# Kernel optimization log

Measured on AMD Instinct MI355X. Metric: run time of the kernel, lower is better.

The kernel has to match this reference:

```python
import jax, jax.numpy as jnp
import numpy as np
from jax import lax

B, N, G, K, D = 16, 8192, 256, 64, 256
DEPTH, H, HID, PH = 4, 8, 1024, 128
EPS = 1e-5
BN_SCALE = float(1.0 / np.sqrt(1.0 + 1e-5))  # BatchNorm eval, running mean 0 / var 1


def setup_inputs() -> dict:
    key = jax.random.key(0)
    ks = iter(jax.random.split(key, 48))
    def rn(shape, s=0.02):
        return jax.random.normal(next(ks), shape, jnp.float32) * s
    z = lambda *s: jnp.zeros(s, jnp.float32)
    o = lambda *s: jnp.ones(s, jnp.float32)
    return dict(
        x=jax.random.normal(next(ks), (B, N, 3), jnp.float32),
        enc_w1=rn((3, 128)), enc_b1=z(128), enc_bn1_g=o(128), enc_bn1_b=z(128),
        enc_w2=rn((128, 256)), enc_b2=z(256),
        enc_w3=rn((512, 512)), enc_b3=z(512), enc_bn2_g=o(512), enc_bn2_b=z(512),
        enc_w4=rn((512, D)), enc_b4=z(D),
        cls_token=rn((1, 1, D)), cls_pos=rn((1, 1, D)),
        pos_w1=rn((3, 128)), pos_b1=z(128), pos_w2=rn((128, D)), pos_b2=z(D),
        ln1_g=o(DEPTH, D), ln1_b=z(DEPTH, D),
        qkv_w=rn((DEPTH, D, 3 * D)),
        proj_w=rn((DEPTH, D, D)), proj_b=z(DEPTH, D),
        ln2_g=o(DEPTH, D), ln2_b=z(DEPTH, D),
        fc1_w=rn((DEPTH, D, HID)), fc1_b=z(DEPTH, HID),
        fc2_w=rn((DEPTH, HID, D)), fc2_b=z(DEPTH, D),
        norm_g=o(D), norm_b=z(D),
        head_w1=rn((D + 3, PH)), head_b1=z(PH), head_w2=rn((PH, 1)), head_b2=z(1),
    )


def layernorm(t, g, b):
    m = jnp.mean(t, -1, keepdims=True)
    v = jnp.mean((t - m) ** 2, -1, keepdims=True)
    return (t - m) / jnp.sqrt(v + EPS) * g + b


def fps(xyz, num_group):
    # farthest point sampling; deterministic start at index 0 (torch uses randint)
    Bb, Nn, _ = xyz.shape
    def body(i, st):
        dist, far, idxs = st
        idxs = idxs.at[:, i].set(far)
        cen = jnp.take_along_axis(xyz, far[:, None, None], axis=1)  # (B,1,3)
        d = jnp.sum((xyz - cen) ** 2, -1)
        dist = jnp.minimum(dist, d)
        far = jnp.argmax(dist, axis=1).astype(jnp.int32)
        return (dist, far, idxs)
    st0 = (jnp.full((Bb, Nn), 1e10, jnp.float32),
           jnp.zeros((Bb,), jnp.int32),
           jnp.zeros((Bb, num_group), jnp.int32))
    _, _, idxs = lax.fori_loop(0, num_group, body, st0)
    centers = jnp.take_along_axis(xyz, idxs[..., None], axis=1)  # (B,G,3)
    return centers, idxs


def knn(xyz, centers, k):
    # squared-distance cdist (same argsort order as p=2) + topk smallest
    c2 = jnp.sum(centers ** 2, -1)[:, :, None]
    x2 = jnp.sum(xyz ** 2, -1)[:, None, :]
    d2 = c2 + x2 - 2.0 * jnp.einsum('bgd,bnd->bgn', centers, xyz)  # (B,G,N)
    idx = lax.top_k(-d2, k)[1]  # (B,G,k)
    neigh = jax.vmap(lambda p, i: p[i])(xyz, idx)  # (B,G,k,3)
    return idx, neigh


def _forward(x, enc_w1, enc_b1, enc_bn1_g, enc_bn1_b, enc_w2, enc_b2,
             enc_w3, enc_b3, enc_bn2_g, enc_bn2_b, enc_w4, enc_b4,
             cls_token, cls_pos, pos_w1, pos_b1, pos_w2, pos_b2,
             ln1_g, ln1_b, qkv_w, proj_w, proj_b, ln2_g, ln2_b,
             fc1_w, fc1_b, fc2_w, fc2_b, norm_g, norm_b,
             head_w1, head_b1, head_w2, head_b2):
    Bb, Nn, _ = x.shape
    # grouping is @torch.no_grad() in the original -> stop_gradient
    pts = lax.stop_gradient(x)
    centers, _ = fps(pts, G)
    idx, neigh = knn(pts, centers, K)
    neigh = neigh - centers[:, :, None, :]  # (B,G,K,3) centered

    # PointNet encoder (kernel-size-1 convs == matmuls; BN eval with unit stats)
    pg = neigh.reshape(Bb * G, K, 3)
    h = pg @ enc_w1 + enc_b1                                # (BG,K,128)
    h = jax.nn.relu(h * enc_bn1_g * BN_SCALE + enc_bn1_b)
    h = h @ enc_w2 + enc_b2                                 # (BG,K,256)
    gmax = jnp.max(h, axis=1, keepdims=True)                # (BG,1,256)
    h = jnp.concatenate([jnp.broadcast_to(gmax, h.shape), h], -1)  # (BG,K,512)
    h = h @ enc_w3 + enc_b3
    h = jax.nn.relu(h * enc_bn2_g * BN_SCALE + enc_bn2_b)
    h = h @ enc_w4 + enc_b4                                 # (BG,K,D)
    tokens = jnp.max(h, axis=1).reshape(Bb, G, D)

    pos = jax.nn.gelu(centers @ pos_w1 + pos_b1, approximate=False) @ pos_w2 + pos_b2
    xt = jnp.concatenate([jnp.broadcast_to(cls_token, (Bb, 1, D)), tokens], 1)
    pt = jnp.concatenate([jnp.broadcast_to(cls_pos, (Bb, 1, D)), pos], 1)

    scale = (D // H) ** -0.5
    for l in range(DEPTH):
        xi = xt + pt  # pos added before every block
        h1 = layernorm(xi, ln1_g[l], ln1_b[l])
        qkv = (h1 @ qkv_w[l]).reshape(Bb, G + 1, 3, H, D // H).transpose(2, 0, 3, 1, 4)
        q, k_, v = qkv[0], qkv[1], qkv[2]
        attn = jax.nn.softmax(jnp.einsum('bhnd,bhmd->bhnm', q, k_) * scale, -1)
        o = jnp.einsum('bhnm,bhmd->bhnd', attn, v).transpose(0, 2, 1, 3).reshape(Bb, G + 1, D)
        xi = xi + o @ proj_w[l] + proj_b[l]
        h2 = layernorm(xi, ln2_g[l], ln2_b[l])
        xi = xi + jax.nn.gelu(h2 @ fc1_w[l] + fc1_b[l], approximate=False) @ fc2_w[l] + fc2_b[l]
        xt = xi
    xt = layernorm(xt, norm_g, norm_b)

    gfeat = xt[:, 1:, :]  # (B,G,D)
    concat = jnp.concatenate(
        [jnp.broadcast_to(gfeat[:, :, None, :], (Bb, G, K, D)), neigh], -1)  # (B,G,K,D+3)
    lg = (jax.nn.relu(concat @ head_w1 + head_b1) @ head_w2 + head_b2)[..., 0]  # (B,G,K)

    # scatter-mean per-point logits over original N points
    flat_i = idx.reshape(Bb, G * K)
    flat_v = lg.reshape(Bb, G * K)
    sums = jax.vmap(lambda v, i: jax.ops.segment_sum(v, i, num_segments=N))(flat_v, flat_i)
    cnts = jax.vmap(lambda i: jax.ops.segment_sum(jnp.ones(i.shape, jnp.float32), i, num_segments=N))(flat_i)
    return sums / jnp.maximum(cnts, 1.0)  # (B,N)


def reference(x, enc_w1, enc_b1, enc_bn1_g, enc_bn1_b, enc_w2, enc_b2,
              enc_w3, enc_b3, enc_bn2_g, enc_bn2_b, enc_w4, enc_b4,
              cls_token, cls_pos, pos_w1, pos_b1, pos_w2, pos_b2,
              ln1_g, ln1_b, qkv_w, proj_w, proj_b, ln2_g, ln2_b,
              fc1_w, fc1_b, fc2_w, fc2_b, norm_g, norm_b,
              head_w1, head_b1, head_w2, head_b2):
    return _forward(x, enc_w1, enc_b1, enc_bn1_g, enc_bn1_b, enc_w2, enc_b2,
                    enc_w3, enc_b3, enc_bn2_g, enc_bn2_b, enc_w4, enc_b4,
                    cls_token, cls_pos, pos_w1, pos_b1, pos_w2, pos_b2,
                    ln1_g, ln1_b, qkv_w, proj_w, proj_b, ln2_g, ln2_b,
                    fc1_w, fc1_b, fc2_w, fc2_b, norm_g, norm_b,
                    head_w1, head_b1, head_w2, head_b2)
```

## Files before the change

### kernel.cpp

```cpp
#include <hip/hip_runtime.h>
#include <hip/hip_bf16.h>

#define B_ 16
#define N_ 8192
#define G_ 256
#define K_ 64
#define D_ 256
#define HID_ 1024
#define EPS_ 1e-5f

typedef __attribute__((ext_vector_type(8))) short bf16x8;
typedef __attribute__((ext_vector_type(4))) float f32x4;

__device__ __forceinline__ float bf16_to_f32(unsigned short u){
  unsigned int v = ((unsigned int)u) << 16;
  return __uint_as_float(v);
}
__device__ __forceinline__ unsigned short f32_to_bf16(float f){
  unsigned int u = __float_as_uint(f);
  unsigned int r = (u + 0x7FFFu + ((u >> 16) & 1u)) >> 16;
  return (unsigned short)r;
}
__device__ __forceinline__ unsigned short bf16h(float a){
  __hip_bfloat16 h = __float2bfloat16(a);
  union { __hip_bfloat16 h; unsigned short u; } cv; cv.h = h; return cv.u;
}
__device__ __forceinline__ unsigned int pk_bf16(float a, float b){
  __hip_bfloat162 h = __float22bfloat162_rn(make_float2(a, b));
  union { __hip_bfloat162 h; unsigned int u; } cv; cv.h = h; return cv.u;
}
__device__ __forceinline__ float gelu_exact(float v){
  return 0.5f * v * (1.0f + erff(v * 0.70710678118654752440f));
}

template<int CTRL>
__device__ __forceinline__ unsigned long long dpp64(unsigned long long k){
  int lo = (int)(unsigned int)k;
  int hi = (int)(unsigned int)(k >> 32);
  int dlo = __builtin_amdgcn_update_dpp(lo, lo, CTRL, 0xF, 0xF, false);
  int dhi = __builtin_amdgcn_update_dpp(hi, hi, CTRL, 0xF, 0xF, false);
  return (((unsigned long long)(unsigned int)dhi) << 32) | (unsigned int)dlo;
}
__device__ __forceinline__ unsigned long long bcast64(unsigned long long k, int lane){
  unsigned int lo = (unsigned int)__builtin_amdgcn_readlane((int)(unsigned int)k, lane);
  unsigned int hi = (unsigned int)__builtin_amdgcn_readlane((int)(unsigned int)(k >> 32), lane);
  return (((unsigned long long)hi) << 32) | lo;
}
__device__ __forceinline__ unsigned long long wave_max64(unsigned long long k){
  unsigned long long t;
  t = dpp64<0x111>(k); if (t > k) k = t;
  t = dpp64<0x112>(k); if (t > k) k = t;
  t = dpp64<0x114>(k); if (t > k) k = t;
  t = dpp64<0x118>(k); if (t > k) k = t;
  t = dpp64<0x142>(k); if (t > k) k = t;
  t = dpp64<0x143>(k); if (t > k) k = t;
  return bcast64(k, 63);
}
__device__ __forceinline__ unsigned long long wave_min64(unsigned long long k){
  unsigned long long t;
  t = dpp64<0x111>(k); if (t < k) k = t;
  t = dpp64<0x112>(k); if (t < k) k = t;
  t = dpp64<0x114>(k); if (t < k) k = t;
  t = dpp64<0x118>(k); if (t < k) k = t;
  t = dpp64<0x142>(k); if (t < k) k = t;
  t = dpp64<0x143>(k); if (t < k) k = t;
  return bcast64(k, 63);
}
__device__ __forceinline__ unsigned long long red8_max64(unsigned long long k){
  unsigned long long t;
  t = dpp64<0x111>(k); if (t > k) k = t;
  t = dpp64<0x112>(k); if (t > k) k = t;
  t = dpp64<0x114>(k); if (t > k) k = t;
  return bcast64(k, 7);
}
__device__ __forceinline__ unsigned long long red4_min64(unsigned long long k){
  unsigned long long t;
  t = dpp64<0x111>(k); if (t < k) k = t;
  t = dpp64<0x112>(k); if (t < k) k = t;
  return bcast64(k, 3);
}

__device__ __forceinline__ void packHi(const float* __restrict__ W, unsigned short* __restrict__ hi,
                                       int f, int N, int ksBits){
  int j = f & 7, lane = (f >> 3) & 63;
  int ks = (f >> 9) & ((1 << ksBits) - 1);
  int nt = f >> (9 + ksBits);
  int k = ks * 32 + ((lane >> 4) & 3) * 8 + j, c = nt * 16 + (lane & 15);
  hi[f] = f32_to_bf16(W[(size_t)k * N + c]);
}

__global__ __launch_bounds__(512) void prep_fps_kernel(
    const float* __restrict__ x, float* __restrict__ centers,
    const float* __restrict__ w1, const float* __restrict__ b1,
    const float* __restrict__ g1, const float* __restrict__ bb1,
    const float* __restrict__ w3, const float* __restrict__ b3,
    const float* __restrict__ g2, const float* __restrict__ bb2,
    const float* __restrict__ enc_w2, const float* __restrict__ enc_w4,
    const float* __restrict__ qkv_w, const float* __restrict__ proj_w,
    const float* __restrict__ fc1_w, const float* __restrict__ fc2_w,
    float* __restrict__ w1f, float* __restrict__ b1f, float* __restrict__ b3f,
    unsigned short* __restrict__ w2ph, unsigned short* __restrict__ w2pl,
    unsigned short* __restrict__ w3ph, unsigned short* __restrict__ w4ph,
    unsigned short* __restrict__ qkvPh, unsigned short* __restrict__ projPh,
    unsigned short* __restrict__ fc1Ph, unsigned short* __restrict__ fc2Ph,
    unsigned short* __restrict__ w3tp)
{
  const float S = 0.99999500003749968f;
  int blk = blockIdx.x, tid = threadIdx.x;

  if (blk >= 17){
    int f = (blk - 17) * 512 + tid;
    if (f < 32768){
      int j = f & 7, lane = (f >> 3) & 63, ks = (f >> 9) & 3, nt = f >> 11;
      int k = ks * 32 + ((lane >> 4) & 3) * 8 + j, c = nt * 16 + (lane & 15);
      float v = enc_w2[(size_t)k * 256 + c];
      unsigned short h = f32_to_bf16(v);
      w2ph[f] = h; w2pl[f] = f32_to_bf16(v - bf16_to_f32(h));
    } else if (f < 163840){
      f -= 32768;
      int j = f & 7, lane = (f >> 3) & 63, ks = (f >> 9) & 7, nt = f >> 12;
      int k = ks * 32 + ((lane >> 4) & 3) * 8 + j, c = nt * 16 + (lane & 15);
      w3ph[f] = f32_to_bf16(w3[(size_t)(256 + k) * 512 + c] * g2[c] * S);
    } else if (f < 294912){
      f -= 163840;
      packHi(enc_w4, w4ph, f, 256, 4);
    } else if (f < 1081344){
      f -= 294912;
      int l = f / 196608, fl = f - l * 196608;
      packHi(qkv_w + (size_t)l * 196608, qkvPh + (size_t)l * 196608, fl, 768, 3);
    } else if (f < 1343488){
      f -= 1081344;
      int l = f >> 16, fl = f & 65535;
      packHi(proj_w + (size_t)l * 65536, projPh + (size_t)l * 65536, fl, 256, 3);
    } else if (f < 2392064){
      f -= 1343488;
      int l = f >> 18, fl = f & 262143;
      packHi(fc1_w + (size_t)l * 262144, fc1Ph + (size_t)l * 262144, fl, 1024, 3);
    } else if (f < 3440640){
      f -= 2392064;
      int l = f >> 18, fl = f & 262143;
      packHi(fc2_w + (size_t)l * 262144, fc2Ph + (size_t)l * 262144, fl, 256, 5);
    } else {
      f -= 3440640;
      int j = f & 7, lane = (f >> 3) & 63, ks = (f >> 9) & 7, nt = f >> 12;
      int k = ks * 32 + ((lane >> 4) & 3) * 8 + j, c = nt * 16 + (lane & 15);
      w3tp[f] = f32_to_bf16(w3[(size_t)k * 512 + c] * g2[c] * S);
    }
    return;
  }
  if (blk == 16){
    if (tid < 384) w1f[tid] = w1[tid] * g1[tid & 127] * S;
    if (tid < 128) b1f[tid] = b1[tid] * g1[tid] * S + bb1[tid];
    b3f[tid] = b3[tid] * g2[tid] * S + bb2[tid];
    return;
  }

  int b = blk;
  const float* xb = x + (size_t)b * N_ * 3;
  int lane = tid & 63, wave = tid >> 6;
  float px[16], py[16], pz[16], dist[16];
#pragma unroll
  for (int j = 0; j < 16; j++){
    int p = tid + j * 512;
    px[j] = xb[p*3+0]; py[j] = xb[p*3+1]; pz[j] = xb[p*3+2];
    dist[j] = 1e10f;
  }
  __shared__ unsigned long long slotK[2][8];
  __shared__ float slotC[2][8][4];
  float cx = xb[0], cy = xb[1], cz = xb[2];
  for (int i = 0; i < G_; i++){
    if (tid == 0){
      float* cp = centers + ((size_t)b * G_ + i) * 3;
      cp[0] = cx; cp[1] = cy; cp[2] = cz;
    }
    float bestv = -1.0f; int bestj = 0;
#pragma unroll
    for (int j = 0; j < 16; j++){
      float dx = __fadd_rn(px[j], -cx);
      float dy = __fadd_rn(py[j], -cy);
      float dz = __fadd_rn(pz[j], -cz);
      float d  = __fadd_rn(__fadd_rn(__fmul_rn(dx,dx), __fmul_rn(dy,dy)), __fmul_rn(dz,dz));
      float dm = fminf(dist[j], d);
      dist[j] = dm;
      if (dm > bestv){ bestv = dm; bestj = j; }
    }
    unsigned int pid = (unsigned int)(tid + bestj * 512);
    unsigned long long key = (((unsigned long long)__float_as_uint(bestv)) << 32) | (unsigned long long)(~pid);
    key = wave_max64(key);
    int par = i & 1;
    unsigned int wpid = ~(unsigned int)key;
    if (lane == (int)(wpid & 63)){
      int jj = (int)(wpid >> 9);
      float fx = px[0], fy = py[0], fz = pz[0];
#pragma unroll
      for (int j = 1; j < 16; j++) if (jj == j){ fx = px[j]; fy = py[j]; fz = pz[j]; }
      slotK[par][wave] = key;
      slotC[par][wave][0] = fx; slotC[par][wave][1] = fy; slotC[par][wave][2] = fz;
    }
    __syncthreads();
    if (i + 1 < G_){
      unsigned long long k2 = slotK[par][lane & 7];
      k2 = red8_max64(k2);
      unsigned int gpid = ~(unsigned int)k2;
      int s = (int)((gpid & 511u) >> 6);
      cx = slotC[par][s][0]; cy = slotC[par][s][1]; cz = slotC[par][s][2];
    }
  }
}

__global__ __launch_bounds__(256) void knn_kernel(const float* __restrict__ x, const float* __restrict__ centers,
                                                  int* __restrict__ knn_idx, float* __restrict__ neigh)
{
  int blk = blockIdx.x, b = blk >> 8;
  const float* xb = x + (size_t)b * N_ * 3;
  const float* cc = centers + (size_t)blk * 3;
  int tid = threadIdx.x, lane = tid & 63, wave = tid >> 6;
  float c0 = cc[0], c1 = cc[1], c2v = cc[2];
  float c2s = __fadd_rn(__fadd_rn(__fmul_rn(c0,c0), __fmul_rn(c1,c1)), __fmul_rn(c2v,c2v));
  float d[32];
#pragma unroll
  for (int j = 0; j < 32; j++){
    int p = tid + j * 256;
    float x0 = xb[p*3+0], x1 = xb[p*3+1], x2 = xb[p*3+2];
    float xs = __fadd_rn(__fadd_rn(__fmul_rn(x0,x0), __fmul_rn(x1,x1)), __fmul_rn(x2,x2));
    float dt = __fadd_rn(__fadd_rn(__fmul_rn(c0,x0), __fmul_rn(c1,x1)), __fmul_rn(c2v,x2));
    d[j] = __fadd_rn(__fadd_rn(c2s, xs), -__fmul_rn(2.0f, dt));
  }
  const float FINF = __int_as_float(0x7F800000);
  float lmin = FINF; unsigned int lp = 0xFFFFFFFFu;
#pragma unroll
  for (int j = 0; j < 32; j++){ if (d[j] < lmin){ lmin = d[j]; lp = (unsigned int)(tid + j*256); } }
  __shared__ unsigned long long wred[2][4];
  for (int r = 0; r < K_; r++){
    unsigned int u = __float_as_uint(lmin);
    u = (u & 0x80000000u) ? ~u : (u | 0x80000000u);
    unsigned long long key = (((unsigned long long)u) << 32) | (unsigned long long)lp;
    key = wave_min64(key);
    int cur = r & 1;
    if (lane == 0) wred[cur][wave] = key;
    __syncthreads();
    unsigned long long m = red4_min64(wred[cur][lane & 3]);
    unsigned int p = (unsigned int)(m & 0xFFFFFFFFull);
    if (tid == (p & 255u)){
      knn_idx[(size_t)blk * K_ + r] = (int)p;
      float* np_ = neigh + ((size_t)blk * K_ + r) * 3;
      np_[0] = __fadd_rn(xb[p*3+0], -c0);
      np_[1] = __fadd_rn(xb[p*3+1], -c1);
      np_[2] = __fadd_rn(xb[p*3+2], -c2v);
      lmin = FINF; lp = 0xFFFFFFFFu;
#pragma unroll
      for (int j = 0; j < 32; j++){
        if ((unsigned int)(tid + j*256) == p) d[j] = FINF;
        if (d[j] < lmin){ lmin = d[j]; lp = (unsigned int)(tid + j*256); }
      }
    }
  }
}

__global__ __launch_bounds__(256, 2) void encoder_kernel(
    const float* __restrict__ neigh,
    const float* __restrict__ w1f, const float* __restrict__ b1f,
    const unsigned short* __restrict__ w2ph, const unsigned short* __restrict__ w2pl,
    const float* __restrict__ b2,
    const float* __restrict__ b3f,
    const unsigned short* __restrict__ w3ph, const unsigned short* __restrict__ w3tp,
    const unsigned short* __restrict__ w4ph,
    const float* __restrict__ b4,
    float* __restrict__ tokens)
{
  __shared__ __align__(16) unsigned short sH1[64 * 136];
  __shared__ __align__(16) unsigned short sH2[64 * 264];
  __shared__ __align__(16) float sShared[256];
  float (*sNeigh)[4] = (float(*)[4])sShared;
  unsigned short* sGmaxBf = (unsigned short*)sShared;

  int tid  = threadIdx.x;
  int wave = tid >> 6, lane = tid & 63, quad = lane >> 4, lrow = lane & 15;
  size_t gid = blockIdx.x;

  if (tid < 192) sNeigh[tid / 3][tid % 3] = neigh[gid * 192 + tid];
  __syncthreads();

  for (int e = tid; e < 8192; e += 256){
    int r = e >> 7, c = e & 127;
    float v = fmaf(sNeigh[r][2], w1f[256 + c], fmaf(sNeigh[r][1], w1f[128 + c], fmaf(sNeigh[r][0], w1f[c], b1f[c])));
    sH1[r * 136 + c] = bf16h(fmaxf(v, 0.0f));
  }
  __syncthreads();

  {
    f32x4 acc[4][4];
    const f32x4 z = {0.f, 0.f, 0.f, 0.f};
#pragma unroll
    for (int mt = 0; mt < 4; mt++)
#pragma unroll
      for (int nl = 0; nl < 4; nl++) acc[mt][nl] = z;
#pragma unroll
    for (int ks = 0; ks < 4; ks++){
      bf16x8 af[4];
#pragma unroll
      for (int mt = 0; mt < 4; mt++)
        af[mt] = *(const bf16x8*)&sH1[(mt*16 + lrow)*136 + ks*32 + quad*8];
#pragma unroll
      for (int nl = 0; nl < 4; nl++){
        size_t bo = (((size_t)(wave*4 + nl)*4 + ks)*64 + lane)*8;
        bf16x8 bh = *(const bf16x8*)&w2ph[bo];
        bf16x8 bl = *(const bf16x8*)&w2pl[bo];
#pragma unroll
        for (int mt = 0; mt < 4; mt++){
          acc[mt][nl] = __builtin_amdgcn_mfma_f32_16x16x32_bf16(af[mt], bh, acc[mt][nl], 0, 0, 0);
          acc[mt][nl] = __builtin_amdgcn_mfma_f32_16x16x32_bf16(af[mt], bl, acc[mt][nl], 0, 0, 0);
        }
      }
    }
#pragma unroll
    for (int nl = 0; nl < 4; nl++){
      int col = wave*64 + nl*16 + lrow;
      float bias = b2[col];
#pragma unroll
      for (int mt = 0; mt < 4; mt++)
#pragma unroll
        for (int rg = 0; rg < 4; rg++)
          sH2[(mt*16 + quad*4 + rg)*264 + col] = bf16h(acc[mt][nl][rg] + bias);
    }
  }
  __syncthreads();

  {
    float mx = -3.4e38f;
#pragma unroll 8
    for (int r = 0; r < 64; r++) mx = fmaxf(mx, bf16_to_f32(sH2[r*264 + tid]));
    sGmaxBf[tid] = bf16h(mx);
  }
  __syncthreads();

  f32x4 acc4[4][4];
  {
    const f32x4 z = {0.f, 0.f, 0.f, 0.f};
#pragma unroll
    for (int mt = 0; mt < 4; mt++)
#pragma unroll
      for (int nl = 0; nl < 4; nl++) acc4[mt][nl] = z;
  }
  for (int cc = 0; cc < 4; cc++){
    f32x4 acc3[4][2], accg[2];
    {
      const f32x4 z = {0.f, 0.f, 0.f, 0.f};
#pragma unroll
      for (int mt = 0; mt < 4; mt++){ acc3[mt][0] = z; acc3[mt][1] = z; }
      accg[0] = z; accg[1] = z;
    }
#pragma unroll
    for (int ks = 0; ks < 8; ks++){
      bf16x8 gf = *(const bf16x8*)&sGmaxBf[ks*32 + quad*8];
#pragma unroll
      for (int nl = 0; nl < 2; nl++){
        int nt = cc*8 + wave*2 + nl;
        size_t bo = (((size_t)nt*8 + ks)*64 + lane)*8;
        bf16x8 bh = *(const bf16x8*)&w3tp[bo];
        accg[nl] = __builtin_amdgcn_mfma_f32_16x16x32_bf16(gf, bh, accg[nl], 0, 0, 0);
      }
    }
#pragma unroll
    for (int ks = 0; ks < 8; ks++){
      bf16x8 af[4];
#pragma unroll
      for (int mt = 0; mt < 4; mt++)
        af[mt] = *(const bf16x8*)&sH2[(mt*16 + lrow)*264 + ks*32 + quad*8];
#pragma unroll
      for (int nl = 0; nl < 2; nl++){
        int nt = cc*8 + wave*2 + nl;
        size_t bo = (((size_t)nt*8 + ks)*64 + lane)*8;
        bf16x8 bh = *(const bf16x8*)&w3ph[bo];
#pragma unroll
        for (int mt = 0; mt < 4; mt++)
          acc3[mt][nl] = __builtin_amdgcn_mfma_f32_16x16x32_bf16(af[mt], bh, acc3[mt][nl], 0, 0, 0);
      }
    }
    __syncthreads();
#pragma unroll
    for (int nl = 0; nl < 2; nl++){
      int cl = wave*32 + nl*16 + lrow;
      int c  = cc*128 + cl;
      float bb = b3f[c];
#pragma unroll
      for (int mt = 0; mt < 4; mt++)
#pragma unroll
        for (int rg = 0; rg < 4; rg++)
          sH1[(mt*16 + quad*4 + rg)*136 + cl] = bf16h(fmaxf(acc3[mt][nl][rg] + accg[nl][rg] + bb, 0.0f));
    }
    __syncthreads();
#pragma unroll
    for (int ks = 0; ks < 4; ks++){
      bf16x8 af[4];
#pragma unroll
      for (int mt = 0; mt < 4; mt++)
        af[mt] = *(const bf16x8*)&sH1[(mt*16 + lrow)*136 + ks*32 + quad*8];
#pragma unroll
      for (int nl = 0; nl < 4; nl++){
        int nt = wave*4 + nl;
        size_t bo = (((size_t)nt*16 + cc*4 + ks)*64 + lane)*8;
        bf16x8 bh = *(const bf16x8*)&w4ph[bo];
#pragma unroll
        for (int mt = 0; mt < 4; mt++)
          acc4[mt][nl] = __builtin_amdgcn_mfma_f32_16x16x32_bf16(af[mt], bh, acc4[mt][nl], 0, 0, 0);
      }
    }
  }

#pragma unroll
  for (int nl = 0; nl < 4; nl++){
    float mx = -3.4e38f;
#pragma unroll
    for (int mt = 0; mt < 4; mt++)
#pragma unroll
      for (int rg = 0; rg < 4; rg++) mx = fmaxf(mx, acc4[mt][nl][rg]);
    mx = fmaxf(mx, __shfl_xor(mx, 16));
    mx = fmaxf(mx, __shfl_xor(mx, 32));
    if (quad == 0){
      int col = wave*64 + nl*16 + lrow;
      tokens[gid * 256 + col] = mx + b4[col];
    }
  }
}

__global__ __launch_bounds__(128) void pos_ln_kernel(
    const float* __restrict__ centers, const float* __restrict__ tokens,
    const float* __restrict__ cls_token, const float* __restrict__ cls_pos,
    const float* __restrict__ pw1, const float* __restrict__ pb1,
    const float* __restrict__ pw2, const float* __restrict__ pb2,
    const float* __restrict__ lng, const float* __restrict__ lnb,
    float* __restrict__ pt, float* __restrict__ xi, float* __restrict__ lnbuf)
{
  __shared__ float hS[128];
  __shared__ float red[2][2];
  int row = blockIdx.x;
  int b = row / 257, n = row - b * 257;
  int tid = threadIdx.x;
  size_t ro = (size_t)row * 256;
  float u0, u1;
  if (n == 0){
    float p0 = cls_pos[tid], p1 = cls_pos[128 + tid];
    u0 = cls_token[tid] + p0; u1 = cls_token[128 + tid] + p1;
    pt[ro + tid] = p0; pt[ro + 128 + tid] = p1;
  } else {
    int g = n - 1;
    const float* c = centers + ((size_t)b * 256 + g) * 3;
    float h = fmaf(c[2], pw1[256 + tid], fmaf(c[1], pw1[128 + tid], fmaf(c[0], pw1[tid], pb1[tid])));
    hS[tid] = gelu_exact(h);
    __syncthreads();
    const float* tok = tokens + ((size_t)b * 256 + g) * 256;
    float s0 = pb2[tid], s1 = pb2[128 + tid];
#pragma unroll 4
    for (int k = 0; k < 128; k++){
      s0 = fmaf(hS[k], pw2[(size_t)k * 256 + tid], s0);
      s1 = fmaf(hS[k], pw2[(size_t)k * 256 + 128 + tid], s1);
    }
    pt[ro + tid] = s0; pt[ro + 128 + tid] = s1;
    u0 = tok[tid] + s0; u1 = tok[128 + tid] + s1;
  }
  float s = u0 + u1, q = u0*u0 + u1*u1;
#pragma unroll
  for (int o = 32; o; o >>= 1){ s += __shfl_down(s, o); q += __shfl_down(q, o); }
  int wv = tid >> 6;
  if ((tid & 63) == 0){ red[0][wv] = s; red[1][wv] = q; }
  __syncthreads();
  float m  = (red[0][0] + red[0][1]) * (1.0f / 256.0f);
  float var = (red[1][0] + red[1][1]) * (1.0f / 256.0f) - m * m;
  float rs = 1.0f / sqrtf(var + EPS_);
  xi[ro + tid] = u0; xi[ro + 128 + tid] = u1;
  lnbuf[ro + tid] = (u0 - m) * rs * lng[tid] + lnb[tid];
  lnbuf[ro + 128 + tid] = (u1 - m) * rs * lng[128 + tid] + lnb[128 + tid];
}

template<int ACT>
__global__ __launch_bounds__(256) void mfma_gemm(
    const float* __restrict__ A, const unsigned short* __restrict__ Bh,
    const float* __restrict__ bias, float* __restrict__ C, int M, int K, int N)
{
  __shared__ __align__(16) unsigned short sA[64 * 72];
  int tid = threadIdx.x;
  int wave = tid >> 6, lane = tid & 63, quad = lane >> 4, lrow = lane & 15;
  int row0 = blockIdx.x * 64;
  int col0 = blockIdx.y * 128;
  int ksTotal = K >> 5;
  f32x4 acc[4][2];
  const f32x4 z = {0.f, 0.f, 0.f, 0.f};
#pragma unroll
  for (int mt = 0; mt < 4; mt++){ acc[mt][0] = z; acc[mt][1] = z; }

  for (int k0 = 0; k0 < K; k0 += 64){
#pragma unroll
    for (int i = 0; i < 4; i++){
      int e = tid + i * 256;
      int r = e >> 4, c4 = (e & 15) * 4;
      int gr = row0 + r;
      float4 v = make_float4(0.f,0.f,0.f,0.f);
      if (gr < M) v = *(const float4*)(A + (size_t)gr * K + k0 + c4);
      unsigned int* dst = (unsigned int*)&sA[r * 72 + c4];
      dst[0] = pk_bf16(v.x, v.y); dst[1] = pk_bf16(v.z, v.w);
    }
    __syncthreads();
    int ksBase = k0 >> 5;
#pragma unroll
    for (int ks = 0; ks < 2; ks++){
      bf16x8 af[4];
#pragma unroll
      for (int mt = 0; mt < 4; mt++)
        af[mt] = *(const bf16x8*)&sA[(mt*16 + lrow)*72 + ks*32 + quad*8];
#pragma unroll
      for (int nl = 0; nl < 2; nl++){
        int nt = (col0 >> 4) + wave*2 + nl;
        size_t bo = (((size_t)nt * ksTotal + ksBase + ks)*64 + lane)*8;
        bf16x8 bh = *(const bf16x8*)&Bh[bo];
#pragma unroll
        for (int mt = 0; mt < 4; mt++)
          acc[mt][nl] = __builtin_amdgcn_mfma_f32_16x16x32_bf16(af[mt], bh, acc[mt][nl], 0, 0, 0);
      }
    }
    __syncthreads();
  }
#pragma unroll
  for (int nl = 0; nl < 2; nl++){
    int c = col0 + wave*32 + nl*16 + lrow;
    float bc = bias ? bias[c] : 0.0f;
#pragma unroll
    for (int mt = 0; mt < 4; mt++)
#pragma unroll
      for (int rg = 0; rg < 4; rg++){
        int r = row0 + mt*16 + quad*4 + rg;
        if (r < M){
          float v = acc[mt][nl][rg] + bc;
          if (ACT == 1) v = gelu_exact(v);
          C[(size_t)r * N + c] = v;
        }
      }
  }
}

__global__ __launch_bounds__(256) void mfma_gemm_ln(
    const float* __restrict__ A, const unsigned short* __restrict__ Bh,
    const float* __restrict__ bias, const float* __restrict__ res,
    const float* __restrict__ ptb,
    float* __restrict__ C, float* __restrict__ xiOut, float* __restrict__ lnOut,
    const float* __restrict__ lng, const float* __restrict__ lnb, int M, int K)
{
  __shared__ __align__(16) unsigned short sA[64 * 72];
  __shared__ float sRed[2][64][4];
  int tid = threadIdx.x;
  int wave = tid >> 6, lane = tid & 63, quad = lane >> 4, lrow = lane & 15;
  int row0 = blockIdx.x * 64;
  int ksTotal = K >> 5;
  f32x4 acc[4][4];
  const f32x4 z = {0.f, 0.f, 0.f, 0.f};
#pragma unroll
  for (int mt = 0; mt < 4; mt++)
#pragma unroll
    for (int nl = 0; nl < 4; nl++) acc[mt][nl] = z;

  for (int k0 = 0; k0 < K; k0 += 64){
#pragma unroll
    for (int i = 0; i < 4; i++){
      int e = tid + i * 256;
      int r = e >> 4, c4 = (e & 15) * 4;
      int gr = row0 + r;
      float4 v = make_float4(0.f,0.f,0.f,0.f);
      if (gr < M) v = *(const float4*)(A + (size_t)gr * K + k0 + c4);
      unsigned int* dst = (unsigned int*)&sA[r * 72 + c4];
      dst[0] = pk_bf16(v.x, v.y); dst[1] = pk_bf16(v.z, v.w);
    }
    __syncthreads();
    int ksBase = k0 >> 5;
#pragma unroll
    for (int ks = 0; ks < 2; ks++){
      bf16x8 af[4];
#pragma unroll
      for (int mt = 0; mt < 4; mt++)
        af[mt] = *(const bf16x8*)&sA[(mt*16 + lrow)*72 + ks*32 + quad*8];
#pragma unroll
      for (int nl = 0; nl < 4; nl++){
        int nt = wave*4 + nl;
        size_t bo = (((size_t)nt * ksTotal + ksBase + ks)*64 + lane)*8;
        bf16x8 bh = *(const bf16x8*)&Bh[bo];
#pragma unroll
        for (int mt = 0; mt < 4; mt++)
          acc[mt][nl] = __builtin_amdgcn_mfma_f32_16x16x32_bf16(af[mt], bh, acc[mt][nl], 0, 0, 0);
      }
    }
    __syncthreads();
  }
#pragma unroll
  for (int nl = 0; nl < 4; nl++){
    int c = wave*64 + nl*16 + lrow;
    float bc = bias[c];
#pragma unroll
    for (int mt = 0; mt < 4; mt++)
#pragma unroll
      for (int rg = 0; rg < 4; rg++){
        int r = row0 + mt*16 + quad*4 + rg;
        if (r < M){
          float v = acc[mt][nl][rg] + bc + res[(size_t)r * 256 + c];
          C[(size_t)r * 256 + c] = v;
          float u = v;
          if (ptb) u += ptb[(size_t)r * 256 + c];
          acc[mt][nl][rg] = u;
        }
      }
  }
#pragma unroll
  for (int mt = 0; mt < 4; mt++)
#pragma unroll
    for (int rg = 0; rg < 4; rg++){
      int rloc = mt*16 + quad*4 + rg;
      float s = 0.0f, q = 0.0f;
#pragma unroll
      for (int nl = 0; nl < 4; nl++){ float u = acc[mt][nl][rg]; s += u; q += u*u; }
#pragma unroll
      for (int off = 1; off < 16; off <<= 1){ s += __shfl_xor(s, off); q += __shfl_xor(q, off); }
      if (lrow == 0){ sRed[0][rloc][wave] = s; sRed[1][rloc][wave] = q; }
    }
  __syncthreads();
#pragma unroll
  for (int mt = 0; mt < 4; mt++)
#pragma unroll
    for (int rg = 0; rg < 4; rg++){
      int rloc = mt*16 + quad*4 + rg;
      int r = row0 + rloc;
      if (r >= M) continue;
      float s = ((sRed[0][rloc][0] + sRed[0][rloc][1]) + sRed[0][rloc][2]) + sRed[0][rloc][3];
      float q = ((sRed[1][rloc][0] + sRed[1][rloc][1]) + sRed[1][rloc][2]) + sRed[1][rloc][3];
      float m  = s * (1.0f / 256.0f);
      float var = q * (1.0f / 256.0f) - m * m;
      float rs = 1.0f / sqrtf(var + EPS_);
#pragma unroll
      for (int nl = 0; nl < 4; nl++){
        int c = wave*64 + nl*16 + lrow;
        float u = acc[mt][nl][rg];
        lnOut[(size_t)r * 256 + c] = (u - m) * rs * lng[c] + lnb[c];
        if (xiOut) xiOut[(size_t)r * 256 + c] = u;
      }
    }
}

__global__ __launch_bounds__(256) void attn_kernel(const float* __restrict__ qkv, float* __restrict__ obuf)
{
  int bh = blockIdx.x;
  int b = bh >> 3, h = bh & 7;
  int tid = threadIdx.x;
  int qi = tid >> 2, kp = tid & 3;
  int qrow = blockIdx.y * 64 + qi;
  bool act = qrow < 257;
  __shared__ float kS[128][33];
  __shared__ float vS[128][33];
  const float* qb = qkv + (size_t)b * 257 * 768;
  float q[32], o[32];
  float mrun = -3.4e38f, l = 0.0f;
  if (act){
    const float* qr = qb + (size_t)qrow * 768 + h * 32;
#pragma unroll
    for (int j = 0; j < 32; j++){ q[j] = qr[j]; o[j] = 0.0f; }
  }
  const float scale = 0.17677669529663687f;
  for (int m0 = 0; m0 < 257; m0 += 128){
    int cnt = min(128, 257 - m0);
    for (int e = tid; e < cnt * 32; e += 256){
      int mm = e >> 5, j = e & 31;
      const float* rowp = qb + (size_t)(m0 + mm) * 768 + h * 32;
      kS[mm][j] = rowp[256 + j];
      vS[mm][j] = rowp[512 + j];
    }
    __syncthreads();
    if (act){
      for (int mm = kp; mm < cnt; mm += 4){
        float s = 0.0f;
#pragma unroll
        for (int j = 0; j < 32; j++) s = fmaf(q[j], kS[mm][j], s);
        s *= scale;
        float nm = fmaxf(mrun, s);
        float alpha = expf(mrun - nm);
        float p = expf(s - nm);
        l = fmaf(l, alpha, p);
#pragma unroll
        for (int j = 0; j < 32; j++) o[j] = fmaf(p, vS[mm][j], o[j] * alpha);
        mrun = nm;
      }
    }
    __syncthreads();
  }
  if (act){
#pragma unroll
    for (int msk = 1; msk <= 2; msk <<= 1){
      float m2 = __shfl_xor(mrun, msk);
      float l2 = __shfl_xor(l, msk);
      float nm = fmaxf(mrun, m2);
      float a1 = expf(mrun - nm), a2 = expf(m2 - nm);
      l = l * a1 + l2 * a2;
#pragma unroll
      for (int j = 0; j < 32; j++){
        float o2 = __shfl_xor(o[j], msk);
        o[j] = o[j] * a1 + o2 * a2;
      }
      mrun = nm;
    }
    if (kp == 0){
      float inv = 1.0f / l;
      float* orow = obuf + (size_t)(b * 257 + qrow) * 256 + h * 32;
#pragma unroll
      for (int j = 0; j < 32; j++) orow[j] = o[j] * inv;
    }
  }
}

__global__ __launch_bounds__(256) void head_kernel(
    const float* __restrict__ gfeat, const float* __restrict__ neigh, const int* __restrict__ knn_idx,
    const float* __restrict__ w1, const float* __restrict__ b1,
    const float* __restrict__ w2, const float* __restrict__ b2,
    float* __restrict__ sums, float* __restrict__ cnts)
{
  int blk = blockIdx.x, b = blk >> 8;
  __shared__ float xS[256];
  __shared__ float nS[64][4];
  __shared__ float partH[2][128];
  __shared__ float sharedH[128];
  __shared__ float w2S[128];
  __shared__ float wtail[3][128];
  int tid = threadIdx.x;
  xS[tid] = gfeat[((size_t)b * 257 + 1 + (blk & 255)) * 256 + tid];
  if (tid < 192) nS[tid / 3][tid % 3] = neigh[(size_t)blk * 192 + tid];
  if (tid < 128){
    w2S[tid] = w2[tid];
    wtail[0][tid] = w1[256 * 128 + tid];
    wtail[1][tid] = w1[257 * 128 + tid];
    wtail[2][tid] = w1[258 * 128 + tid];
  }
  __syncthreads();
  {
    int half = tid >> 7, j = tid & 127;
    float s = 0.0f;
#pragma unroll 8
    for (int k = 0; k < 128; k++) s = fmaf(xS[half * 128 + k], w1[(size_t)(half * 128 + k) * 128 + j], s);
    partH[half][j] = s;
  }
  __syncthreads();
  if (tid < 128) sharedH[tid] = partH[0][tid] + partH[1][tid] + b1[tid];
  __syncthreads();
  int r = tid >> 2, q = tid & 3;
  float n0 = nS[r][0], n1 = nS[r][1], n2 = nS[r][2];
  float s = 0.0f;
#pragma unroll
  for (int j0 = 0; j0 < 32; j0++){
    int j = q * 32 + j0;
    float h = fmaf(n2, wtail[2][j], fmaf(n1, wtail[1][j], fmaf(n0, wtail[0][j], sharedH[j])));
    s = fmaf(fmaxf(h, 0.0f), w2S[j], s);
  }
  s += __shfl_xor(s, 1);
  s += __shfl_xor(s, 2);
  if (q == 0){
    float lg = s + b2[0];
    int p = knn_idx[(size_t)blk * K_ + r];
    atomicAdd(&sums[(size_t)b * N_ + p], lg);
    atomicAdd(&cnts[(size_t)b * N_ + p], 1.0f);
  }
}

__global__ void finalize_kernel(const float* __restrict__ sums, const float* __restrict__ cnts, float* __restrict__ out)
{
  int i = blockIdx.x * 256 + threadIdx.x;
  out[i] = sums[i] / fmaxf(cnts[i], 1.0f);
}

extern "C" void kernel_launch(void* const* d_in, const int* in_sizes, int n_in,
                              void* d_out, int out_size, void* d_ws, size_t ws_size,
                              hipStream_t stream)
{
  (void)in_sizes; (void)n_in; (void)out_size; (void)ws_size;
  const float* x        = (const float*)d_in[0];
  const float* enc_w1   = (const float*)d_in[1];
  const float* enc_b1   = (const float*)d_in[2];
  const float* enc_bn1g = (const float*)d_in[3];
  const float* enc_bn1b = (const float*)d_in[4];
  const float* enc_w2   = (const float*)d_in[5];
  const float* enc_b2   = (const float*)d_in[6];
  const float* enc_w3   = (const float*)d_in[7];
  const float* enc_b3   = (const float*)d_in[8];
  const float* enc_bn2g = (const float*)d_in[9];
  const float* enc_bn2b = (const float*)d_in[10];
  const float* enc_w4   = (const float*)d_in[11];
  const float* enc_b4   = (const float*)d_in[12];
  const float* cls_tok  = (const float*)d_in[13];
  const float* cls_pos  = (const float*)d_in[14];
  const float* pos_w1   = (const float*)d_in[15];
  const float* pos_b1   = (const float*)d_in[16];
  const float* pos_w2   = (const float*)d_in[17];
  const float* pos_b2   = (const float*)d_in[18];
  const float* ln1_g    = (const float*)d_in[19];
  const float* ln1_b    = (const float*)d_in[20];
  const float* qkv_w    = (const float*)d_in[21];
  const float* proj_w   = (const float*)d_in[22];
  const float* proj_b   = (const float*)d_in[23];
  const float* ln2_g    = (const float*)d_in[24];
  const float* ln2_b    = (const float*)d_in[25];
  const float* fc1_w    = (const float*)d_in[26];
  const float* fc1_b    = (const float*)d_in[27];
  const float* fc2_w    = (const float*)d_in[28];
  const float* fc2_b    = (const float*)d_in[29];
  const float* norm_g   = (const float*)d_in[30];
  const float* norm_b   = (const float*)d_in[31];
  const float* head_w1  = (const float*)d_in[32];
  const float* head_b1  = (const float*)d_in[33];
  const float* head_w2  = (const float*)d_in[34];
  const float* head_b2  = (const float*)d_in[35];

  float* ws = (float*)d_ws;
  size_t off = 0;
  auto alloc = [&](size_t n)->float*{ float* p = ws + off; off += (n + 63) & ~(size_t)63; return p; };

  float* centers = alloc((size_t)B_ * G_ * 3);
  float* w1f     = alloc(384);
  float* b1f     = alloc(128);
  float* b3f     = alloc(512);
  unsigned short* w2ph = (unsigned short*)alloc(16384);
  unsigned short* w2pl = (unsigned short*)alloc(16384);
  unsigned short* w3ph = (unsigned short*)alloc(65536);
  unsigned short* w3tp = (unsigned short*)alloc(65536);
  unsigned short* w4ph = (unsigned short*)alloc(65536);
  unsigned short* qkvPh = (unsigned short*)alloc(393216);
  unsigned short* projPh = (unsigned short*)alloc(131072);
  unsigned short* fc1Ph = (unsigned short*)alloc(524288);
  unsigned short* fc2Ph = (unsigned short*)alloc(524288);
  float* tokens  = alloc((size_t)B_ * G_ * D_);
  float* neigh   = alloc((size_t)B_ * G_ * K_ * 3);
  int*   knn_idx = (int*)alloc((size_t)B_ * G_ * K_);
  float* pt      = alloc((size_t)B_ * 257 * D_);
  float* xt      = alloc((size_t)B_ * 257 * D_);
  float* xi      = alloc((size_t)B_ * 257 * D_);
  float* lnbuf   = alloc((size_t)B_ * 257 * D_);
  float* obuf    = alloc((size_t)B_ * 257 * D_);
  float* bigbuf  = alloc((size_t)B_ * 257 * HID_);
  float* gfeat   = alloc((size_t)B_ * 257 * D_);
  float* sums    = alloc((size_t)B_ * N_);
  float* cnts    = alloc((size_t)B_ * N_);

  hipMemsetAsync(sums, 0, (size_t)2 * B_ * N_ * sizeof(float), stream);

  prep_fps_kernel<<<6993, 512, 0, stream>>>(x, centers,
      enc_w1, enc_b1, enc_bn1g, enc_bn1b, enc_w3, enc_b3, enc_bn2g, enc_bn2b,
      enc_w2, enc_w4, qkv_w, proj_w, fc1_w, fc2_w,
      w1f, b1f, b3f, w2ph, w2pl, w3ph, w4ph, qkvPh, projPh, fc1Ph, fc2Ph, w3tp);

  knn_kernel<<<B_ * G_, 256, 0, stream>>>(x, centers, knn_idx, neigh);
  encoder_kernel<<<B_ * G_, 256, 0, stream>>>(neigh, w1f, b1f, w2ph, w2pl, enc_b2,
                                              b3f, w3ph, w3tp, w4ph, enc_b4, tokens);
  pos_ln_kernel<<<B_ * 257, 128, 0, stream>>>(centers, tokens, cls_tok, cls_pos,
                                              pos_w1, pos_b1, pos_w2, pos_b2,
                                              ln1_g, ln1_b, pt, xi, lnbuf);
  const int M = B_ * 257;
  for (int l = 0; l < 4; l++){
    mfma_gemm<0><<<dim3(65, 6), 256, 0, stream>>>(lnbuf, qkvPh + (size_t)l*196608, nullptr, bigbuf, M, 256, 768);
    attn_kernel<<<dim3(B_ * 8, 5), 256, 0, stream>>>(bigbuf, obuf);
    mfma_gemm_ln<<<65, 256, 0, stream>>>(obuf, projPh + (size_t)l*65536, proj_b + l*256, xi, nullptr,
                                         xi, nullptr, lnbuf, ln2_g + l*256, ln2_b + l*256, M, 256);
    mfma_gemm<1><<<dim3(65, 8), 256, 0, stream>>>(lnbuf, fc1Ph + (size_t)l*262144, fc1_b + l*1024, bigbuf, M, 256, 1024);
    if (l < 3){
      mfma_gemm_ln<<<65, 256, 0, stream>>>(bigbuf, fc2Ph + (size_t)l*262144, fc2_b + l*256, xi, pt,
                                           xt, xi, lnbuf, ln1_g + (l+1)*256, ln1_b + (l+1)*256, M, 1024);
    } else {
      mfma_gemm_ln<<<65, 256, 0, stream>>>(bigbuf, fc2Ph + (size_t)l*262144, fc2_b + l*256, xi, nullptr,
                                           xt, nullptr, gfeat, norm_g, norm_b, M, 1024);
    }
  }
  head_kernel<<<B_ * G_, 256, 0, stream>>>(gfeat, neigh, knn_idx, head_w1, head_b1, head_w2, head_b2, sums, cnts);
  finalize_kernel<<<(B_ * N_) / 256, 256, 0, stream>>>(sums, cnts, (float*)d_out);
}
```

Baseline: 1.927 ms.

## Store transformer activations in bf16 and read FPS winner coordinates via readlane

Intermediate activation buffers (LN outputs, qkv, attention output, MLP hidden, final features) are now written and read as bf16 instead of fp32. This halves their memory traffic and lets the GEMM A-tile loads copy 8 bf16 values straight into shared memory without converting. The unused xt output store is dropped. In FPS, each lane reads the per-wave winner coordinates as one float4 and picks the global winner with readlane, replacing a dependent shared-memory read. The extra bf16 rounding of activations like qkv and attention output may add some numerical error.

```diff
diff --git a/kernel.cpp b/kernel.cpp
--- a/kernel.cpp
+++ b/kernel.cpp
@@ -24,10 +24,6 @@
 __device__ __forceinline__ unsigned short bf16h(float a){
   __hip_bfloat16 h = __float2bfloat16(a);
   union { __hip_bfloat16 h; unsigned short u; } cv; cv.h = h; return cv.u;
-}
-__device__ __forceinline__ unsigned int pk_bf16(float a, float b){
-  __hip_bfloat162 h = __float22bfloat162_rn(make_float2(a, b));
-  union { __hip_bfloat162 h; unsigned int u; } cv; cv.h = h; return cv.u;
 }
 __device__ __forceinline__ float gelu_exact(float v){
   return 0.5f * v * (1.0f + erff(v * 0.70710678118654752440f));
@@ -166,7 +162,7 @@
     dist[j] = 1e10f;
   }
   __shared__ unsigned long long slotK[2][8];
-  __shared__ float slotC[2][8][4];
+  __shared__ float4 slotC[2][8];
   float cx = xb[0], cy = xb[1], cz = xb[2];
   for (int i = 0; i < G_; i++){
     if (tid == 0){
@@ -195,15 +191,19 @@
 #pragma unroll
       for (int j = 1; j < 16; j++) if (jj == j){ fx = px[j]; fy = py[j]; fz = pz[j]; }
       slotK[par][wave] = key;
-      slotC[par][wave][0] = fx; slotC[par][wave][1] = fy; slotC[par][wave][2] = fz;
+      slotC[par][wave] = make_float4(fx, fy, fz, 0.0f);
     }
     __syncthreads();
     if (i + 1 < G_){
-      unsigned long long k2 = slotK[par][lane & 7];
+      int sl = lane & 7;
+      unsigned long long k2 = slotK[par][sl];
+      float4 cc4 = slotC[par][sl];
       k2 = red8_max64(k2);
       unsigned int gpid = ~(unsigned int)k2;
       int s = (int)((gpid & 511u) >> 6);
-      cx = slotC[par][s][0]; cy = slotC[par][s][1]; cz = slotC[par][s][2];
+      cx = __uint_as_float((unsigned int)__builtin_amdgcn_readlane((int)__float_as_uint(cc4.x), s));
+      cy = __uint_as_float((unsigned int)__builtin_amdgcn_readlane((int)__float_as_uint(cc4.y), s));
+      cz = __uint_as_float((unsigned int)__builtin_amdgcn_readlane((int)__float_as_uint(cc4.z), s));
     }
   }
 }
@@ -430,7 +430,7 @@
     const float* __restrict__ pw1, const float* __restrict__ pb1,
     const float* __restrict__ pw2, const float* __restrict__ pb2,
     const float* __restrict__ lng, const float* __restrict__ lnb,
-    float* __restrict__ pt, float* __restrict__ xi, float* __restrict__ lnbuf)
+    float* __restrict__ pt, float* __restrict__ xi, unsigned short* __restrict__ lnbuf)
 {
   __shared__ float hS[128];
   __shared__ float red[2][2];
@@ -469,14 +469,14 @@
   float var = (red[1][0] + red[1][1]) * (1.0f / 256.0f) - m * m;
   float rs = 1.0f / sqrtf(var + EPS_);
   xi[ro + tid] = u0; xi[ro + 128 + tid] = u1;
-  lnbuf[ro + tid] = (u0 - m) * rs * lng[tid] + lnb[tid];
-  lnbuf[ro + 128 + tid] = (u1 - m) * rs * lng[128 + tid] + lnb[128 + tid];
+  lnbuf[ro + tid] = bf16h((u0 - m) * rs * lng[tid] + lnb[tid]);
+  lnbuf[ro + 128 + tid] = bf16h((u1 - m) * rs * lng[128 + tid] + lnb[128 + tid]);
 }
 
 template<int ACT>
 __global__ __launch_bounds__(256) void mfma_gemm(
-    const float* __restrict__ A, const unsigned short* __restrict__ Bh,
-    const float* __restrict__ bias, float* __restrict__ C, int M, int K, int N)
+    const unsigned short* __restrict__ A, const unsigned short* __restrict__ Bh,
+    const float* __restrict__ bias, unsigned short* __restrict__ C, int M, int K, int N)
 {
   __shared__ __align__(16) unsigned short sA[64 * 72];
   int tid = threadIdx.x;
@@ -491,14 +491,13 @@
 
   for (int k0 = 0; k0 < K; k0 += 64){
 #pragma unroll
-    for (int i = 0; i < 4; i++){
+    for (int i = 0; i < 2; i++){
       int e = tid + i * 256;
-      int r = e >> 4, c4 = (e & 15) * 4;
+      int r = e >> 3, c8 = (e & 7) * 8;
       int gr = row0 + r;
-      float4 v = make_float4(0.f,0.f,0.f,0.f);
-      if (gr < M) v = *(const float4*)(A + (size_t)gr * K + k0 + c4);
-      unsigned int* dst = (unsigned int*)&sA[r * 72 + c4];
-      dst[0] = pk_bf16(v.x, v.y); dst[1] = pk_bf16(v.z, v.w);
+      bf16x8 v = {0,0,0,0,0,0,0,0};
+      if (gr < M) v = *(const bf16x8*)(A + (size_t)gr * K + k0 + c8);
+      *(bf16x8*)&sA[r * 72 + c8] = v;
     }
     __syncthreads();
     int ksBase = k0 >> 5;
@@ -532,17 +531,17 @@
         if (r < M){
           float v = acc[mt][nl][rg] + bc;
           if (ACT == 1) v = gelu_exact(v);
-          C[(size_t)r * N + c] = v;
+          C[(size_t)r * N + c] = bf16h(v);
         }
       }
   }
 }
 
 __global__ __launch_bounds__(256) void mfma_gemm_ln(
-    const float* __restrict__ A, const unsigned short* __restrict__ Bh,
+    const unsigned short* __restrict__ A, const unsigned short* __restrict__ Bh,
     const float* __restrict__ bias, const float* __restrict__ res,
     const float* __restrict__ ptb,
-    float* __restrict__ C, float* __restrict__ xiOut, float* __restrict__ lnOut,
+    float* __restrict__ C, float* __restrict__ xiOut, unsigned short* __restrict__ lnOut,
     const float* __restrict__ lng, const float* __restrict__ lnb, int M, int K)
 {
   __shared__ __align__(16) unsigned short sA[64 * 72];
@@ -560,14 +559,13 @@
 
   for (int k0 = 0; k0 < K; k0 += 64){
 #pragma unroll
-    for (int i = 0; i < 4; i++){
+    for (int i = 0; i < 2; i++){
       int e = tid + i * 256;
-      int r = e >> 4, c4 = (e & 15) * 4;
+      int r = e >> 3, c8 = (e & 7) * 8;
       int gr = row0 + r;
-      float4 v = make_float4(0.f,0.f,0.f,0.f);
-      if (gr < M) v = *(const float4*)(A + (size_t)gr * K + k0 + c4);
-      unsigned int* dst = (unsigned int*)&sA[r * 72 + c4];
-      dst[0] = pk_bf16(v.x, v.y); dst[1] = pk_bf16(v.z, v.w);
+      bf16x8 v = {0,0,0,0,0,0,0,0};
+      if (gr < M) v = *(const bf16x8*)(A + (size_t)gr * K + k0 + c8);
+      *(bf16x8*)&sA[r * 72 + c8] = v;
     }
     __syncthreads();
     int ksBase = k0 >> 5;
@@ -600,7 +598,7 @@
         int r = row0 + mt*16 + quad*4 + rg;
         if (r < M){
           float v = acc[mt][nl][rg] + bc + res[(size_t)r * 256 + c];
-          C[(size_t)r * 256 + c] = v;
+          if (C) C[(size_t)r * 256 + c] = v;
           float u = v;
           if (ptb) u += ptb[(size_t)r * 256 + c];
           acc[mt][nl][rg] = u;
@@ -636,13 +634,13 @@
       for (int nl = 0; nl < 4; nl++){
         int c = wave*64 + nl*16 + lrow;
         float u = acc[mt][nl][rg];
-        lnOut[(size_t)r * 256 + c] = (u - m) * rs * lng[c] + lnb[c];
+        lnOut[(size_t)r * 256 + c] = bf16h((u - m) * rs * lng[c] + lnb[c]);
         if (xiOut) xiOut[(size_t)r * 256 + c] = u;
       }
     }
 }
 
-__global__ __launch_bounds__(256) void attn_kernel(const float* __restrict__ qkv, float* __restrict__ obuf)
+__global__ __launch_bounds__(256) void attn_kernel(const unsigned short* __restrict__ qkv, unsigned short* __restrict__ obuf)
 {
   int bh = blockIdx.x;
   int b = bh >> 3, h = bh & 7;
@@ -652,22 +650,22 @@
   bool act = qrow < 257;
   __shared__ float kS[128][33];
   __shared__ float vS[128][33];
-  const float* qb = qkv + (size_t)b * 257 * 768;
+  const unsigned short* qb = qkv + (size_t)b * 257 * 768;
   float q[32], o[32];
   float mrun = -3.4e38f, l = 0.0f;
   if (act){
-    const float* qr = qb + (size_t)qrow * 768 + h * 32;
-#pragma unroll
-    for (int j = 0; j < 32; j++){ q[j] = qr[j]; o[j] = 0.0f; }
+    const unsigned short* qr = qb + (size_t)qrow * 768 + h * 32;
+#pragma unroll
+    for (int j = 0; j < 32; j++){ q[j] = bf16_to_f32(qr[j]); o[j] = 0.0f; }
   }
   const float scale = 0.17677669529663687f;
   for (int m0 = 0; m0 < 257; m0 += 128){
     int cnt = min(128, 257 - m0);
     for (int e = tid; e < cnt * 32; e += 256){
       int mm = e >> 5, j = e & 31;
-      const float* rowp = qb + (size_t)(m0 + mm) * 768 + h * 32;
-      kS[mm][j] = rowp[256 + j];
-      vS[mm][j] = rowp[512 + j];
+      const unsigned short* rowp = qb + (size_t)(m0 + mm) * 768 + h * 32;
+      kS[mm][j] = bf16_to_f32(rowp[256 + j]);
+      vS[mm][j] = bf16_to_f32(rowp[512 + j]);
     }
     __syncthreads();
     if (act){
@@ -704,15 +702,15 @@
     }
     if (kp == 0){
       float inv = 1.0f / l;
-      float* orow = obuf + (size_t)(b * 257 + qrow) * 256 + h * 32;
-#pragma unroll
-      for (int j = 0; j < 32; j++) orow[j] = o[j] * inv;
+      unsigned short* orow = obuf + (size_t)(b * 257 + qrow) * 256 + h * 32;
+#pragma unroll
+      for (int j = 0; j < 32; j++) orow[j] = bf16h(o[j] * inv);
     }
   }
 }
 
 __global__ __launch_bounds__(256) void head_kernel(
-    const float* __restrict__ gfeat, const float* __restrict__ neigh, const int* __restrict__ knn_idx,
+    const unsigned short* __restrict__ gfeat, const float* __restrict__ neigh, const int* __restrict__ knn_idx,
     const float* __restrict__ w1, const float* __restrict__ b1,
     const float* __restrict__ w2, const float* __restrict__ b2,
     float* __restrict__ sums, float* __restrict__ cnts)
@@ -725,7 +723,7 @@
   __shared__ float w2S[128];
   __shared__ float wtail[3][128];
   int tid = threadIdx.x;
-  xS[tid] = gfeat[((size_t)b * 257 + 1 + (blk & 255)) * 256 + tid];
+  xS[tid] = bf16_to_f32(gfeat[((size_t)b * 257 + 1 + (blk & 255)) * 256 + tid]);
   if (tid < 192) nS[tid / 3][tid % 3] = neigh[(size_t)blk * 192 + tid];
   if (tid < 128){
     w2S[tid] = w2[tid];
@@ -832,12 +830,11 @@
   float* neigh   = alloc((size_t)B_ * G_ * K_ * 3);
   int*   knn_idx = (int*)alloc((size_t)B_ * G_ * K_);
   float* pt      = alloc((size_t)B_ * 257 * D_);
-  float* xt      = alloc((size_t)B_ * 257 * D_);
   float* xi      = alloc((size_t)B_ * 257 * D_);
-  float* lnbuf   = alloc((size_t)B_ * 257 * D_);
-  float* obuf    = alloc((size_t)B_ * 257 * D_);
-  float* bigbuf  = alloc((size_t)B_ * 257 * HID_);
-  float* gfeat   = alloc((size_t)B_ * 257 * D_);
+  unsigned short* lnbufB = (unsigned short*)alloc((size_t)B_ * 257 * D_ / 2 + 64);
+  unsigned short* obufB  = (unsigned short*)alloc((size_t)B_ * 257 * D_ / 2 + 64);
+  unsigned short* bigbufB= (unsigned short*)alloc((size_t)B_ * 257 * HID_ / 2 + 64);
+  unsigned short* gfeatB = (unsigned short*)alloc((size_t)B_ * 257 * D_ / 2 + 64);
   float* sums    = alloc((size_t)B_ * N_);
   float* cnts    = alloc((size_t)B_ * N_);
 
@@ -853,22 +850,22 @@
                                               b3f, w3ph, w3tp, w4ph, enc_b4, tokens);
   pos_ln_kernel<<<B_ * 257, 128, 0, stream>>>(centers, tokens, cls_tok, cls_pos,
                                               pos_w1, pos_b1, pos_w2, pos_b2,
-                                              ln1_g, ln1_b, pt, xi, lnbuf);
+                                              ln1_g, ln1_b, pt, xi, lnbufB);
   const int M = B_ * 257;
   for (int l = 0; l < 4; l++){
-    mfma_gemm<0><<<dim3(65, 6), 256, 0, stream>>>(lnbuf, qkvPh + (size_t)l*196608, nullptr, bigbuf, M, 256, 768);
-    attn_kernel<<<dim3(B_ * 8, 5), 256, 0, stream>>>(bigbuf, obuf);
-    mfma_gemm_ln<<<65, 256, 0, stream>>>(obuf, projPh + (size_t)l*65536, proj_b + l*256, xi, nullptr,
-                                         xi, nullptr, lnbuf, ln2_g + l*256, ln2_b + l*256, M, 256);
-    mfma_gemm<1><<<dim3(65, 8), 256, 0, stream>>>(lnbuf, fc1Ph + (size_t)l*262144, fc1_b + l*1024, bigbuf, M, 256, 1024);
+    mfma_gemm<0><<<dim3(65, 6), 256, 0, stream>>>(lnbufB, qkvPh + (size_t)l*196608, nullptr, bigbufB, M, 256, 768);
+    attn_kernel<<<dim3(B_ * 8, 5), 256, 0, stream>>>(bigbufB, obufB);
+    mfma_gemm_ln<<<65, 256, 0, stream>>>(obufB, projPh + (size_t)l*65536, proj_b + l*256, xi, nullptr,
+                                         xi, nullptr, lnbufB, ln2_g + l*256, ln2_b + l*256, M, 256);
+    mfma_gemm<1><<<dim3(65, 8), 256, 0, stream>>>(lnbufB, fc1Ph + (size_t)l*262144, fc1_b + l*1024, bigbufB, M, 256, 1024);
     if (l < 3){
-      mfma_gemm_ln<<<65, 256, 0, stream>>>(bigbuf, fc2Ph + (size_t)l*262144, fc2_b + l*256, xi, pt,
-                                           xt, xi, lnbuf, ln1_g + (l+1)*256, ln1_b + (l+1)*256, M, 1024);
+      mfma_gemm_ln<<<65, 256, 0, stream>>>(bigbufB, fc2Ph + (size_t)l*262144, fc2_b + l*256, xi, pt,
+                                           nullptr, xi, lnbufB, ln1_g + (l+1)*256, ln1_b + (l+1)*256, M, 1024);
     } else {
-      mfma_gemm_ln<<<65, 256, 0, stream>>>(bigbuf, fc2Ph + (size_t)l*262144, fc2_b + l*256, xi, nullptr,
-                                           xt, nullptr, gfeat, norm_g, norm_b, M, 1024);
-    }
-  }
-  head_kernel<<<B_ * G_, 256, 0, stream>>>(gfeat, neigh, knn_idx, head_w1, head_b1, head_w2, head_b2, sums, cnts);
+      mfma_gemm_ln<<<65, 256, 0, stream>>>(bigbufB, fc2Ph + (size_t)l*262144, fc2_b + l*256, xi, nullptr,
+                                           nullptr, nullptr, gfeatB, norm_g, norm_b, M, 1024);
+    }
+  }
+  head_kernel<<<B_ * G_, 256, 0, stream>>>(gfeatB, neigh, knn_idx, head_w1, head_b1, head_w2, head_b2, sums, cnts);
   finalize_kernel<<<(B_ * N_) / 256, 256, 0, stream>>>(sums, cnts, (float*)d_out);
 }
```

After: 1.814 ms. 5.9% less time.
